# Performance work log

Hardware: AMD Instinct MI355X
Metric: run time of the kernel (lower is better)

The kernel has to match this reference:

```python
import jax, jax.numpy as jnp
import numpy as np


def setup_inputs() -> dict:
    key = jax.random.key(0)
    ks = jax.random.split(key, 5)
    B, C, H, W = 4, 256, 64, 64
    Cq = C // 8
    x = jax.random.normal(ks[0], (B, C, H, W), dtype=jnp.float32)
    Wq = jax.random.normal(ks[1], (Cq, C), dtype=jnp.float32) * (1.0 / np.sqrt(C))
    Wk = jax.random.normal(ks[2], (Cq, C), dtype=jnp.float32) * (1.0 / np.sqrt(C))
    Wv = jax.random.normal(ks[3], (C, C), dtype=jnp.float32) * (1.0 / np.sqrt(C))
    bq = jnp.zeros((Cq,), dtype=jnp.float32)
    bk = jnp.zeros((Cq,), dtype=jnp.float32)
    bv = jnp.zeros((C,), dtype=jnp.float32)
    gamma = jnp.ones((1,), dtype=jnp.float32)
    return {"x": x, "Wq": Wq, "bq": bq, "Wk": Wk, "bk": bk, "Wv": Wv, "bv": bv, "gamma": gamma}


def reference(x, Wq, bq, Wk, bk, Wv, bv, gamma):
    B, C, H, W = x.shape
    N = H * W
    xf = x.reshape(B, C, N)                      # (B, C, N)
    # 1x1 convs == per-pixel linear projections over channels
    q = jnp.einsum('dc,bcn->bdn', Wq, xf) + bq[None, :, None]   # (B, C/8, N)
    k = jnp.einsum('dc,bcn->bdn', Wk, xf) + bk[None, :, None]   # (B, C/8, N)
    v = jnp.einsum('dc,bcn->bdn', Wv, xf) + bv[None, :, None]   # (B, C,   N)
    # attention: note original has NO 1/sqrt(d) scaling
    scores = jnp.einsum('bdn,bdm->bnm', q, k)     # (B, N, N)
    attn = jax.nn.softmax(scores, axis=-1)
    out = jnp.einsum('bnm,bdm->bnd', attn, v)     # (B, N, C)
    out = out.transpose(0, 2, 1).reshape(B, C, H, W)
    return gamma * out + x
```

## Files before the change

### kernel.cpp

```cpp
#include <hip/hip_runtime.h>

#define BATCH 4
#define CH    256
#define DQ    32
#define NPIX  4096
#define LOG2E 1.44269504088896340736f

typedef unsigned short u16;
typedef unsigned int   u32;
typedef __attribute__((ext_vector_type(8))) short short8;
typedef __attribute__((ext_vector_type(16))) float f32x16;

__device__ __align__(16) u16 g_wbf[10 * 2 * 8192];
__device__ float g_bias[10 * 32];

__device__ __forceinline__ float b2f(u32 u) {
  union { u32 i; float f; } v; v.i = (u & 0xffffu) << 16; return v.f;
}
__device__ __forceinline__ u16 f2b(float f) {
  union { float f; u32 i; } v; v.f = f;
  u32 x = v.i; x += 0x7fffu + ((x >> 16) & 1u);
  return (u16)(x >> 16);
}
__device__ __forceinline__ float fexp2(float x) {
#if __has_builtin(__builtin_amdgcn_exp2f)
  return __builtin_amdgcn_exp2f(x);
#else
  return __expf(x * 0.69314718055994530942f);
#endif
}
__device__ __forceinline__ u32 cvtpk_bf16(float a, float b) {
  u32 r;
  asm("v_cvt_pk_bf16_f32 %0, %1, %2" : "=v"(r) : "v"(a), "v"(b));
  return r;
}

__device__ __forceinline__ void half_swap(u32 a0, u32 a1, u32 b0, u32 b1,
                                          int hl, uint4& o) {
#if __has_builtin(__builtin_amdgcn_permlane32_swap)
  const auto r0 = __builtin_amdgcn_permlane32_swap((int)a0, (int)b0, false, false);
  const auto r1 = __builtin_amdgcn_permlane32_swap((int)a1, (int)b1, false, false);
  o.x = (u32)r0[0]; o.y = (u32)r1[0]; o.z = (u32)r0[1]; o.w = (u32)r1[1];
#else
  const u32 s0 = hl ? a0 : b0;
  const u32 s1 = hl ? a1 : b1;
  const u32 r0 = (u32)__shfl_xor((int)s0, 32);
  const u32 r1 = (u32)__shfl_xor((int)s1, 32);
  o.x = hl ? r0 : a0; o.y = hl ? r1 : a1;
  o.z = hl ? b0 : r0; o.w = hl ? b1 : r1;
#endif
}

__global__ __launch_bounds__(256) void xprep(
    const float* __restrict__ x, u16* __restrict__ xt_hi, u16* __restrict__ xt_lo,
    const float* __restrict__ Wq, const float* __restrict__ bq,
    const float* __restrict__ Wk, const float* __restrict__ bk,
    const float* __restrict__ Wv, const float* __restrict__ bv)
{
  const int t = threadIdx.x;

  if (blockIdx.z == BATCH) {
    if (blockIdx.y != 0 || blockIdx.x >= 10) return;
    const int jt = blockIdx.x;
    const float* Wsrc; const float* bsrc; int jrow0; float scale = 1.f;
    if (jt == 0)      { Wsrc = Wq; bsrc = bq; jrow0 = 0; scale = LOG2E; }
    else if (jt == 1) { Wsrc = Wk; bsrc = bk; jrow0 = 0; }
    else              { Wsrc = Wv; bsrc = bv; jrow0 = (jt - 2) * 32; }
    u16* wdst = g_wbf + (size_t)jt * 16384;
    for (int i = 0; i < 32; ++i) {
      const int flat = i * 256 + t;
      const int j = flat >> 8, e = flat & 255;
      const float v = Wsrc[(size_t)(jrow0 + j) * CH + e] * scale;
      const u16 hi = f2b(v);
      const u16 lo = f2b(v - b2f(hi));
      const int idx = (((e >> 4) * 2 + ((e >> 3) & 1)) * 32 + j) * 8 + (e & 7);
      wdst[idx] = hi; wdst[8192 + idx] = lo;
    }
    if (t < 32) g_bias[jt * 32 + t] = bsrc[jrow0 + t] * scale;
    return;
  }

  const int nt = blockIdx.x, kb4 = blockIdx.y * 4, b = blockIdx.z;
  const int n0 = nt * 128, c0 = blockIdx.y * 64;
  __shared__ u32 xls[64][129];

  const int tn = t & 127, cp = t >> 7;
  for (int i = 0; i < 32; ++i) {
    const int c = cp + 2 * i;
    const float v = x[((size_t)b * CH + c0 + c) * NPIX + n0 + tn];
    const u16 h = f2b(v);
    const u16 l = f2b(v - b2f(h));
    xls[c][tn] = (u32)h | ((u32)l << 16);
  }
  __syncthreads();

  for (int rep = 0; rep < 4; ++rep) {
    const int id = t + 256 * rep;
    const int kkhl = id >> 7, n = id & 127;
    union { short8 s; uint4 u; } vh, vl;
    #pragma unroll
    for (int j = 0; j < 8; ++j) {
      const u32 p = xls[kkhl * 8 + j][n];
      vh.s[j] = (short)(p & 0xffffu);
      vl.s[j] = (short)(p >> 16);
    }
    const size_t o = ((((size_t)(b * 32 + nt) * 16 + kb4 + (kkhl >> 1)) * 2
                       + (kkhl & 1)) * 128 + n) * 8;
    *(uint4*)(xt_hi + o) = vh.u;
    *(uint4*)(xt_lo + o) = vl.u;
  }
}

__global__ __launch_bounds__(256, 4) void proj(
    const u16* __restrict__ xt_hi, const u16* __restrict__ xt_lo,
    u16* __restrict__ q_t, u16* __restrict__ k_t, u16* __restrict__ v_swz)
{
  const int L = blockIdx.x;
  const int xcd = L & 7, s = L >> 3;
  const int jt = s >> 4;
  const int pair = xcd * 16 + (s & 15);
  const int nt = pair >> 2, b = pair & 3;

  const int t = threadIdx.x;
  const int w = t >> 6, lane = t & 63, hl = lane >> 5, l31 = lane & 31;
  const int nb = w * 32 + l31, n = nt * 128 + nb;

  const u16* __restrict__ wb = g_wbf + (size_t)jt * 16384;
  const size_t xtile = (size_t)(b * 32 + nt) * 16 * 2 * 128 * 8;
  const u16* __restrict__ xh = xt_hi + xtile;
  const u16* __restrict__ xl = xt_lo + xtile;

  f32x16 acc1, acc2;
  #pragma unroll
  for (int r = 0; r < 16; ++r) { acc1[r] = 0.f; acc2[r] = 0.f; }

  #pragma unroll
  for (int kk = 0; kk < 16; ++kk) {
    const int aoff = ((kk * 2 + hl) * 32 + l31) * 8;
    const short8 wah = *(const short8*)(wb + aoff);
    const short8 wal = *(const short8*)(wb + 8192 + aoff);
    const int boff = ((kk * 2 + hl) * 128 + nb) * 8;
    const short8 xbh = *(const short8*)(xh + boff);
    const short8 xbl = *(const short8*)(xl + boff);
    acc1 = __builtin_amdgcn_mfma_f32_32x32x16_bf16(wah, xbh, acc1, 0, 0, 0);
    acc2 = __builtin_amdgcn_mfma_f32_32x32x16_bf16(wah, xbl, acc2, 0, 0, 0);
    acc2 = __builtin_amdgcn_mfma_f32_32x32x16_bf16(wal, xbh, acc2, 0, 0, 0);
  }

  f32x16 accv;
  #pragma unroll
  for (int r = 0; r < 16; ++r)
    accv[r] = acc1[r] + acc2[r]
            + g_bias[jt * 32 + (r & 3) + 8 * (r >> 2) + 4 * hl];

  if (jt <= 1) {
    u16* dst = (jt == 0) ? q_t : k_t;
    #pragma unroll
    for (int r2 = 0; r2 < 4; ++r2) {
      uint2 pk;
      pk.x = (u32)f2b(accv[4 * r2 + 0]) | ((u32)f2b(accv[4 * r2 + 1]) << 16);
      pk.y = (u32)f2b(accv[4 * r2 + 2]) | ((u32)f2b(accv[4 * r2 + 3]) << 16);
      *(uint2*)(dst + ((size_t)b * NPIX + n) * DQ + 4 * hl + 8 * r2) = pk;
    }
  } else {
    const int mc = nt * 4 + w;
    const int kc = (l31 >> 4) & 1, h3 = (l31 >> 3) & 1, j8 = l31 & 7;
    u16* dst = v_swz + (((((size_t)b * 128 + mc) * 8 + (jt - 2)) * 2 + kc) * 2 + h3) * 256 + j8;
    #pragma unroll
    for (int r = 0; r < 16; ++r) {
      const int c5 = (r & 3) + 8 * (r >> 2) + 4 * hl;
      dst[c5 * 8] = f2b(accv[r]);
    }
  }
}

__global__ __launch_bounds__(512, 4) void attn(
    const u16* __restrict__ q_t, const u16* __restrict__ k_t,
    const u16* __restrict__ v_swz, const float* __restrict__ x,
    const float* __restrict__ gamma, float* __restrict__ out)
{
  const int L = blockIdx.x;
  const int xcd = L & 7, slot = L >> 3;
  const int b = xcd >> 1;
  const int nt = slot * 2 + (xcd & 1);
  const int n0 = nt * 32;

  const int t = threadIdx.x;
  const int w = t >> 6, lane = t & 63, hl = lane >> 5, l31 = lane & 31;
  const int g = w >> 1, h = w & 1;

  __shared__ float cbuf[8192];
  __shared__ float lbuf[4][64];

  short8 qf[2];
  #pragma unroll
  for (int kd = 0; kd < 2; ++kd)
    qf[kd] = *(const short8*)(q_t + ((size_t)b * NPIX + n0 + l31) * DQ + kd * 16 + hl * 8);

  f32x16 acc[4];
  #pragma unroll
  for (int c = 0; c < 4; ++c)
    #pragma unroll
    for (int r = 0; r < 16; ++r) acc[c][r] = 0.f;
  float lrun = 0.f;

  const u16* __restrict__ kb = k_t + (size_t)b * NPIX * DQ;
  const u16* __restrict__ vb = v_swz + ((size_t)b * 128) * 8192
                               + h * 4096 + hl * 256 + l31 * 8;

  for (int cc = 0; cc < 32; ++cc) {
    const int mc = g * 32 + cc;

    const short8 kf0 = *(const short8*)(kb + (mc * 32 + l31) * DQ + hl * 8);
    const short8 kf1 = *(const short8*)(kb + (mc * 32 + l31) * DQ + 16 + hl * 8);
    f32x16 st;
    #pragma unroll
    for (int r = 0; r < 16; ++r) st[r] = 0.f;
    st = __builtin_amdgcn_mfma_f32_32x32x16_bf16(kf0, qf[0], st, 0, 0, 0);
    st = __builtin_amdgcn_mfma_f32_32x32x16_bf16(kf1, qf[1], st, 0, 0, 0);

    u32 pk[4][2];
    #pragma unroll
    for (int g4 = 0; g4 < 4; ++g4) {
      const float e0 = fexp2(st[4 * g4 + 0]);
      const float e1 = fexp2(st[4 * g4 + 1]);
      const float e2 = fexp2(st[4 * g4 + 2]);
      const float e3 = fexp2(st[4 * g4 + 3]);
      lrun += (e0 + e1) + (e2 + e3);
      pk[g4][0] = cvtpk_bf16(e0, e1);
      pk[g4][1] = cvtpk_bf16(e2, e3);
    }

    const u16* __restrict__ vpt = vb + (size_t)mc * 8192;
    #pragma unroll
    for (int kc = 0; kc < 2; ++kc) {
      union { uint4 u; short8 s; } bu;
      half_swap(pk[2 * kc][0], pk[2 * kc][1], pk[2 * kc + 1][0], pk[2 * kc + 1][1], hl, bu.u);
      #pragma unroll
      for (int c = 0; c < 4; ++c) {
        const short8 av = *(const short8*)(vpt + (c * 2 + kc) * 512);
        acc[c] = __builtin_amdgcn_mfma_f32_32x32x16_bf16(av, bu.s, acc[c], 0, 0, 0);
      }
    }
  }

  if (h == 0) lbuf[g][lane] = lrun;

  for (int gs = 0; gs < 4; ++gs) {
    __syncthreads();
    if (g == gs) {
      #pragma unroll
      for (int c = 0; c < 4; ++c)
        #pragma unroll
        for (int r = 0; r < 16; ++r) {
          const int ch = (h * 4 + c) * 32 + (r & 3) + 8 * (r >> 2) + 4 * hl;
          const int idx = ch * 32 + l31;
          if (gs == 0) cbuf[idx] = acc[c][r];
          else         cbuf[idx] += acc[c][r];
        }
    }
  }
  __syncthreads();

  const int col = t & 31, chg = t >> 5;
  float l = 0.f;
  #pragma unroll
  for (int gg = 0; gg < 4; ++gg)
    l += lbuf[gg][col] + lbuf[gg][col + 32];
  const float linv = 1.0f / l;
  const float gmv = gamma[0];
  #pragma unroll
  for (int i = 0; i < 16; ++i) {
    const int ch = chg * 16 + i;
    const float cb = cbuf[ch * 32 + col];
    const size_t oidx = ((size_t)b * CH + ch) * NPIX + n0 + col;
    out[oidx] = gmv * cb * linv + x[oidx];
  }
}

extern "C" void kernel_launch(void* const* d_in, const int* in_sizes, int n_in,
                              void* d_out, int out_size, void* d_ws, size_t ws_size,
                              hipStream_t stream) {
  const float* x  = (const float*)d_in[0];
  const float* Wq = (const float*)d_in[1];
  const float* bq = (const float*)d_in[2];
  const float* Wk = (const float*)d_in[3];
  const float* bk = (const float*)d_in[4];
  const float* Wv = (const float*)d_in[5];
  const float* bv = (const float*)d_in[6];
  const float* gm = (const float*)d_in[7];
  float* out = (float*)d_out;

  const size_t qk_elems = (size_t)BATCH * NPIX * DQ;
  const size_t v_elems  = (size_t)BATCH * NPIX * CH;
  const size_t need = (2 * qk_elems + v_elems) * sizeof(u16);
  if (ws_size < need) return;

  u16* q_t   = (u16*)d_ws;
  u16* k_t   = q_t + qk_elems;
  u16* v_swz = k_t + qk_elems;

  u16* xt_hi = (u16*)d_out;
  u16* xt_lo = xt_hi + (size_t)BATCH * NPIX * CH;

  xprep<<<dim3(NPIX / 128, CH / 64, BATCH + 1), 256, 0, stream>>>(
      x, xt_hi, xt_lo, Wq, bq, Wk, bk, Wv, bv);
  proj<<<dim3(32 * 10 * BATCH), 256, 0, stream>>>(xt_hi, xt_lo, q_t, k_t, v_swz);
  attn<<<dim3((NPIX / 32) * BATCH), 512, 0, stream>>>(q_t, k_t, v_swz, x, gm, out);
}
```

Baseline: 160.6 us.

## Double-buffer V tiles into LDS via async global_load_lds prefetch

Each wave now prefetches the next V tile straight into its own LDS double buffer with global_load_lds, while the current tile's QK MFMA and exp work runs. The PV MFMA operands are then read from LDS instead of global memory. The 128KB shared buffer is reused afterwards for the cross-group reduction, and launch bounds drop from 4 to 2 blocks per CU. This trades occupancy and LDS capacity for hiding global V load latency, and the wait relies on a hand-written vmcnt count.

```diff
diff --git a/kernel.cpp b/kernel.cpp
--- a/kernel.cpp
+++ b/kernel.cpp
@@ -33,6 +33,11 @@
   u32 r;
   asm("v_cvt_pk_bf16_f32 %0, %1, %2" : "=v"(r) : "v"(a), "v"(b));
   return r;
+}
+__device__ __forceinline__ void gload_lds16(const u16* gsrc, u16* ldst) {
+  __builtin_amdgcn_global_load_lds(
+      (const __attribute__((address_space(1))) void*)gsrc,
+      (__attribute__((address_space(3))) void*)ldst, 16, 0, 0);
 }
 
 __device__ __forceinline__ void half_swap(u32 a0, u32 a1, u32 b0, u32 b1,
@@ -174,7 +179,7 @@
   }
 }
 
-__global__ __launch_bounds__(512, 4) void attn(
+__global__ __launch_bounds__(512, 2) void attn(
     const u16* __restrict__ q_t, const u16* __restrict__ k_t,
     const u16* __restrict__ v_swz, const float* __restrict__ x,
     const float* __restrict__ gamma, float* __restrict__ out)
@@ -189,8 +194,8 @@
   const int w = t >> 6, lane = t & 63, hl = lane >> 5, l31 = lane & 31;
   const int g = w >> 1, h = w & 1;
 
-  __shared__ float cbuf[8192];
-  __shared__ float lbuf[4][64];
+  __shared__ u16 smem[65536];
+  u16* const vls = smem + w * 8192;
 
   short8 qf[2];
   #pragma unroll
@@ -205,14 +210,30 @@
   float lrun = 0.f;
 
   const u16* __restrict__ kb = k_t + (size_t)b * NPIX * DQ;
-  const u16* __restrict__ vb = v_swz + ((size_t)b * 128) * 8192
-                               + h * 4096 + hl * 256 + l31 * 8;
+  const u16* __restrict__ vsrc = v_swz + ((size_t)b * 128) * 8192
+                                 + h * 4096 + lane * 8;
+
+  {
+    const u16* s0 = vsrc + (size_t)(g * 32) * 8192;
+    #pragma unroll
+    for (int i = 0; i < 8; ++i) gload_lds16(s0 + i * 512, vls + i * 512);
+  }
 
   for (int cc = 0; cc < 32; ++cc) {
     const int mc = g * 32 + cc;
+    const int buf = cc & 1;
 
     const short8 kf0 = *(const short8*)(kb + (mc * 32 + l31) * DQ + hl * 8);
     const short8 kf1 = *(const short8*)(kb + (mc * 32 + l31) * DQ + 16 + hl * 8);
+
+    {
+      const int mcn = g * 32 + ((cc < 31) ? cc + 1 : 31);
+      const u16* sn = vsrc + (size_t)mcn * 8192;
+      u16* dn = vls + (buf ^ 1) * 4096;
+      #pragma unroll
+      for (int i = 0; i < 8; ++i) gload_lds16(sn + i * 512, dn + i * 512);
+    }
+
     f32x16 st;
     #pragma unroll
     for (int r = 0; r < 16; ++r) st[r] = 0.f;
@@ -231,22 +252,37 @@
       pk[g4][1] = cvtpk_bf16(e2, e3);
     }
 
-    const u16* __restrict__ vpt = vb + (size_t)mc * 8192;
+    asm volatile("s_waitcnt vmcnt(8)" ::: "memory");
+    __builtin_amdgcn_sched_barrier(0);
+
+    const u16* vt = vls + buf * 4096;
     #pragma unroll
     for (int kc = 0; kc < 2; ++kc) {
       union { uint4 u; short8 s; } bu;
       half_swap(pk[2 * kc][0], pk[2 * kc][1], pk[2 * kc + 1][0], pk[2 * kc + 1][1], hl, bu.u);
       #pragma unroll
       for (int c = 0; c < 4; ++c) {
-        const short8 av = *(const short8*)(vpt + (c * 2 + kc) * 512);
+        const short8 av = *(const short8*)(vt + (c * 2 + kc) * 512 + hl * 256 + l31 * 8);
         acc[c] = __builtin_amdgcn_mfma_f32_32x32x16_bf16(av, bu.s, acc[c], 0, 0, 0);
       }
     }
   }
 
-  if (h == 0) lbuf[g][lane] = lrun;
-
-  for (int gs = 0; gs < 4; ++gs) {
+  __syncthreads();
+  float* const cbuf = (float*)smem;
+  float* const lbf  = (float*)smem + 8192;
+
+  if (h == 0) lbf[g * 64 + lane] = lrun;
+  if (g == 0) {
+    #pragma unroll
+    for (int c = 0; c < 4; ++c)
+      #pragma unroll
+      for (int r = 0; r < 16; ++r) {
+        const int ch = (h * 4 + c) * 32 + (r & 3) + 8 * (r >> 2) + 4 * hl;
+        cbuf[ch * 32 + l31] = acc[c][r];
+      }
+  }
+  for (int gs = 1; gs < 4; ++gs) {
     __syncthreads();
     if (g == gs) {
       #pragma unroll
@@ -254,9 +290,7 @@
         #pragma unroll
         for (int r = 0; r < 16; ++r) {
           const int ch = (h * 4 + c) * 32 + (r & 3) + 8 * (r >> 2) + 4 * hl;
-          const int idx = ch * 32 + l31;
-          if (gs == 0) cbuf[idx] = acc[c][r];
-          else         cbuf[idx] += acc[c][r];
+          cbuf[ch * 32 + l31] += acc[c][r];
         }
     }
   }
@@ -266,7 +300,7 @@
   float l = 0.f;
   #pragma unroll
   for (int gg = 0; gg < 4; ++gg)
-    l += lbuf[gg][col] + lbuf[gg][col + 32];
+    l += lbf[gg * 64 + col] + lbf[gg * 64 + col + 32];
   const float linv = 1.0f / l;
   const float gmv = gamma[0];
   #pragma unroll
```

Result: slower. 171.4 us (+6.7%).
